# Kernel optimization log

Hardware: AMD Instinct MI355X
Metric: run time of the kernel (lower is better)

The kernel has to match this reference:

```python
import jax, jax.numpy as jnp
import numpy as np

IOU_THR = 0.5
SCORE_THR = 0.05
K = 1000  # fixed NMS candidate budget (padded-ragged replacement for data-dependent shapes)
BBOX_XFORM_CLIP = float(np.log(1000.0 / 16.0))  # torchvision BoxCoder clamp


def setup_inputs() -> dict:
    key = jax.random.key(0)
    k1, k2, k3, k4 = jax.random.split(key, 4)
    B, N, C = 8, 50000, 80
    pred_labels = jax.random.normal(k1, (B, N, C), jnp.float32)
    pred_bboxes = 0.5 * jax.random.normal(k2, (B, N, 4), jnp.float32)
    # anchors: valid xyxy boxes on a ~640px image
    cxy = jax.random.uniform(k3, (B, N, 2), jnp.float32, minval=0.0, maxval=640.0)
    wh = jax.random.uniform(k4, (B, N, 2), jnp.float32, minval=8.0, maxval=128.0)
    anchors = jnp.concatenate([cxy - 0.5 * wh, cxy + 0.5 * wh], axis=-1)
    return {"pred_labels": pred_labels, "pred_bboxes": pred_bboxes, "anchors": anchors}


def _decode_boxes(codes, anchors):
    # torchvision BoxCoder.decode_single with weights (1,1,1,1)
    w = anchors[:, 2] - anchors[:, 0]
    h = anchors[:, 3] - anchors[:, 1]
    cx = anchors[:, 0] + 0.5 * w
    cy = anchors[:, 1] + 0.5 * h
    dx, dy = codes[:, 0], codes[:, 1]
    dw = jnp.minimum(codes[:, 2], BBOX_XFORM_CLIP)
    dh = jnp.minimum(codes[:, 3], BBOX_XFORM_CLIP)
    pcx = dx * w + cx
    pcy = dy * h + cy
    pw = jnp.exp(dw) * w
    ph = jnp.exp(dh) * h
    return jnp.stack([pcx - 0.5 * pw, pcy - 0.5 * ph, pcx + 0.5 * pw, pcy + 0.5 * ph], axis=-1)


def _pairwise_iou(b):
    # b: [K,4] xyxy
    area = (b[:, 2] - b[:, 0]) * (b[:, 3] - b[:, 1])
    lt = jnp.maximum(b[:, None, :2], b[None, :, :2])
    rb = jnp.minimum(b[:, None, 2:], b[None, :, 2:])
    wh = jnp.clip(rb - lt, 0.0)
    inter = wh[..., 0] * wh[..., 1]
    return inter / (area[:, None] + area[None, :] - inter + 1e-9)


def _nms_keep(boxes):
    # boxes already sorted by descending score; greedy suppression
    iou = _pairwise_iou(boxes)
    idx = jnp.arange(K)

    def body(i, keep):
        suppress = (iou[i] > IOU_THR) & (idx > i) & keep[i]
        return keep & ~suppress

    return jax.lax.fori_loop(0, K, body, jnp.ones((K,), bool))


def _decode_image(labels, codes, anchors):
    # labels [N,C], codes [N,4], anchors [N,4]
    probs = jax.nn.sigmoid(labels)
    dt_score = jnp.max(probs, axis=1)
    dt_class = jnp.argmax(probs, axis=1)
    fg = (dt_class != 0) & (dt_score > SCORE_THR)
    masked = jnp.where(fg, dt_score, -1.0)  # background sorts last
    top_s, top_i = jax.lax.top_k(masked, K)
    cls = dt_class[top_i]
    boxes = _decode_boxes(codes[top_i], anchors[top_i])
    keep = _nms_keep(boxes) & (top_s > 0.0)
    out_scores = jnp.where(keep, top_s, 0.0)
    out_boxes = jnp.where(keep[:, None], boxes, 0.0)
    out_cls = jnp.where(keep, cls, -1)
    return out_cls, out_scores, out_boxes, keep


def reference(pred_labels, pred_bboxes, anchors):
    # Padded-ragged analog of the nested_tensor result:
    # category_ids [B,K] int, scores [B,K], bboxes [B,K,4], keep [B,K] validity mask
    return jax.vmap(_decode_image)(pred_labels, pred_bboxes, anchors)
```

## Files before the change

kernel.cpp:

```cpp
#include <hip/hip_runtime.h>
#include <cstdint>
#include <cstddef>

typedef unsigned int u32;
typedef unsigned long long u64;

#define BB   8
#define NN   50000
#define CC   80
#define KTOP 1000
#define CAP  4096
#define NHB  129
#define CLIPV 4.135166556742356f

#define OFF_KEYS 0UL
#define OFF_CLS  1600000UL
#define OFF_HIST 3200000UL
#define OFF_CNT  3204128UL
#define OFF_CAND 3204640UL
#define OFF_TKEY 3466784UL
#define OFF_TIDX 3498784UL
#define OFF_BOX  3530784UL
#define OFF_AREA 3658784UL
#define OFF_MAT  3690784UL
#define OFF_KEEP 4714784UL

__global__ __launch_bounds__(256) void k_scores_u(const float4* __restrict__ labels4,
                                                  u32* __restrict__ keys,
                                                  int* __restrict__ cls,
                                                  u32* __restrict__ ghist) {
    __shared__ float4 tile[64 * 21];
    __shared__ float  pbest[3][64];
    __shared__ int    pcls[3][64];
    __shared__ u32    lhist[NHB];
    int t = threadIdx.x;
    int img = blockIdx.x / 196;
    int blk = blockIdx.x - img * 196;
    size_t img_base = (size_t)img * NN * 20;
    for (int i = t; i < NHB; i += 256) lhist[i] = 0;
    int a = t & 63;
    int q = t >> 6;
#pragma unroll
    for (int tl = 0; tl < 4; ++tl) {
        int na0 = blk * 256 + tl * 64;
        int nv = NN - na0; if (nv > 64) nv = 64; if (nv < 0) nv = 0;
        int lim = nv * 20;
#pragma unroll
        for (int i = 0; i < 5; ++i) {
            int s = i * 256 + t;
            if (s < lim) {
                float4 v = labels4[img_base + (size_t)na0 * 20 + s];
                tile[s + s / 20] = v;
            }
        }
        __syncthreads();
        float best = -1.0e30f; int bc = 0;
        if (a < nv) {
#pragma unroll
            for (int j = 0; j < 5; ++j) {
                float4 v = tile[a * 21 + q * 5 + j];
                int c = q * 20 + j * 4;
                if (v.x > best) { best = v.x; bc = c; }
                if (v.y > best) { best = v.y; bc = c + 1; }
                if (v.z > best) { best = v.z; bc = c + 2; }
                if (v.w > best) { best = v.w; bc = c + 3; }
            }
            if (q > 0) { pbest[q - 1][a] = best; pcls[q - 1][a] = bc; }
        }
        __syncthreads();
        if (q == 0 && a < nv) {
#pragma unroll
            for (int r = 0; r < 3; ++r) {
                float pb = pbest[r][a];
                if (pb > best) { best = pb; bc = pcls[r][a]; }
            }
            int g = img * NN + na0 + a;
            float score = 1.0f / (1.0f + expf(-best));
            bool fg = (bc != 0) && (score > 0.05f);
            u32 key = fg ? __float_as_uint(score) : 0u;
            keys[g] = key;
            cls[g] = bc;
            u32 kb = key >> 16;
            u32 idx = (kb >= 0x3F00u) ? (kb - 0x3F00u) : 128u;
            atomicAdd(&lhist[idx], 1u);
        }
        __syncthreads();
    }
    for (int i = t; i < NHB; i += 256) {
        u32 c = lhist[i];
        if (c) atomicAdd(&ghist[img * NHB + i], c);
    }
}

__global__ __launch_bounds__(256) void k_gather(const u32* __restrict__ keys,
                                                const u32* __restrict__ ghist,
                                                u32* __restrict__ cnt,
                                                u64* __restrict__ cand) {
    __shared__ u32 wsum[4];
    __shared__ u32 bbase;
    __shared__ u32 sT16;
    __shared__ u32 wtot;
    int t = threadIdx.x;
    int img = blockIdx.x / 196;
    int blk = blockIdx.x - img * 196;

    u32 v = 0;
    if (t < 128) v = ghist[img * NHB + (127 - t)];
    u32 incl = v;
#pragma unroll
    for (int d = 1; d < 64; d <<= 1) {
        u32 up = __shfl_up(incl, (unsigned)d);
        if ((t & 63) >= d) incl += up;
    }
    if (t == 63) wtot = incl;
    __syncthreads();
    if (t >= 64 && t < 128) incl += wtot;
    if (t < 128) {
        u32 excl = incl - v;
        if (excl < KTOP && incl >= KTOP) sT16 = 0x3F00u + 127u - (u32)t;
    }
    if (t == 127 && incl < KTOP) sT16 = 0x3F00u;
    __syncthreads();
    u32 T16 = sT16;

    int n = blk * 256 + t;
    u32 key = 0; bool pass = false;
    if (n < NN) {
        key = keys[img * NN + n];
        pass = (key >> 16) >= T16;
    }
    u64 mask = __ballot(pass);
    int lane = t & 63, wid = t >> 6;
    u32 prefix = (u32)__popcll(mask & ((1ull << lane) - 1ull));
    if (lane == 0) wsum[wid] = (u32)__popcll(mask);
    __syncthreads();
    if (t == 0) {
        u32 s0 = wsum[0], s1 = wsum[1], s2 = wsum[2], s3 = wsum[3];
        u32 tot = s0 + s1 + s2 + s3;
        bbase = tot ? atomicAdd(&cnt[img * 16], tot) : 0u;
        wsum[0] = 0; wsum[1] = s0; wsum[2] = s0 + s1; wsum[3] = s0 + s1 + s2;
    }
    __syncthreads();
    if (pass) {
        u32 pos = bbase + wsum[wid] + prefix;
        if (pos < CAP)
            cand[(size_t)img * CAP + pos] = ((u64)key << 32) | (u32)(~(u32)n);
    }
}

__global__ __launch_bounds__(256) void k_sortA(u64* __restrict__ cand,
                                               const u32* __restrict__ cnt) {
    __shared__ u64 sm[1024];
    int b = blockIdx.x >> 2;
    int c = blockIdx.x & 3;
    int tid = threadIdx.x;
    int m = (int)min(cnt[b * 16], (u32)CAP);
    int base = c * 1024;
    u64* cp = cand + (size_t)b * CAP;
    for (int i = tid; i < 1024; i += 256) {
        int g = base + i;
        sm[i] = (g < m) ? cp[g] : 0ull;
    }
    __syncthreads();
    for (int k = 2; k <= 1024; k <<= 1)
        for (int j = k >> 1; j > 0; j >>= 1) {
            for (int i = tid; i < 1024; i += 256) {
                int ixj = i ^ j;
                if (ixj > i) {
                    bool desc = (((base + i) & k) == 0);
                    u64 x = sm[i], y = sm[ixj];
                    if (desc ? (x < y) : (x > y)) { sm[i] = y; sm[ixj] = x; }
                }
            }
            __syncthreads();
        }
    for (int i = tid; i < 1024; i += 256) cp[base + i] = sm[i];
}

__global__ __launch_bounds__(512) void k_sortB(const u64* __restrict__ cand,
                                               const float4* __restrict__ codes,
                                               const float4* __restrict__ anchors,
                                               u32* __restrict__ tkey, u32* __restrict__ tidx,
                                               float4* __restrict__ boxes, float* __restrict__ area) {
    __shared__ u64 sm[CAP];
    int b = blockIdx.x, tid = threadIdx.x;
    const u64* cp = cand + (size_t)b * CAP;
    for (int i = tid; i < CAP; i += 512) sm[i] = cp[i];
    __syncthreads();
    for (int k = 2048; k <= 4096; k <<= 1)
        for (int j = k >> 1; j > 0; j >>= 1) {
            for (int i = tid; i < CAP; i += 512) {
                int ixj = i ^ j;
                if (ixj > i) {
                    bool desc = ((i & k) == 0);
                    u64 x = sm[i], y = sm[ixj];
                    if (desc ? (x < y) : (x > y)) { sm[i] = y; sm[ixj] = x; }
                }
            }
            __syncthreads();
        }
#pragma unroll
    for (int r = 0; r < 2; ++r) {
        int i = r * 512 + tid;
        if (i < KTOP) {
            u64 v = sm[i];
            u32 kb = (u32)(v >> 32);
            u32 n = ~(u32)v;
            if (kb == 0u) n = 0u;
            int g = b * KTOP + i;
            tkey[g] = kb; tidx[g] = n;
            float4 a = anchors[(size_t)b * NN + n];
            float4 cc = codes[(size_t)b * NN + n];
            float w = a.z - a.x, h = a.w - a.y;
            float cx = a.x + 0.5f * w, cy = a.y + 0.5f * h;
            float dw = fminf(cc.z, CLIPV), dh = fminf(cc.w, CLIPV);
            float pcx = cc.x * w + cx, pcy = cc.y * h + cy;
            float pw = expf(dw) * w, ph = expf(dh) * h;
            float x0 = pcx - 0.5f * pw, y0 = pcy - 0.5f * ph;
            float x1 = pcx + 0.5f * pw, y1 = pcy + 0.5f * ph;
            boxes[g] = make_float4(x0, y0, x1, y1);
            area[g] = (x1 - x0) * (y1 - y0);
        }
    }
}

__global__ __launch_bounds__(256) void k_mat(const float4* __restrict__ boxes,
                                             const float* __restrict__ area,
                                             u64* __restrict__ mat) {
    __shared__ float4 sb[256];
    __shared__ float  sa[256];
    int bid = blockIdx.x;
    int wc = bid & 3, rc = (bid >> 2) & 3, b = bid >> 4;
    int t = threadIdx.x;
    int j0 = wc * 256;
    int jn = min(256, KTOP - j0);
    if (t < jn) { sb[t] = boxes[b * KTOP + j0 + t]; sa[t] = area[b * KTOP + j0 + t]; }
    __syncthreads();
    if (t >= 250) return;
    int i = rc * 250 + t;
    float4 bi = boxes[b * KTOP + i];
    float ai = area[b * KTOP + i];
    u64 w[4] = {0ull, 0ull, 0ull, 0ull};
    int estart = i - j0 + 1; if (estart < 0) estart = 0;
    for (int e = estart; e < jn; ++e) {
        float4 bj = sb[e];
        float lx = fmaxf(bi.x, bj.x), ly = fmaxf(bi.y, bj.y);
        float rx = fminf(bi.z, bj.z), ry = fminf(bi.w, bj.w);
        float ww = fmaxf(rx - lx, 0.0f), hh = fmaxf(ry - ly, 0.0f);
        float inter = ww * hh;
        float iou = inter / (ai + sa[e] - inter + 1e-9f);
        if (iou > 0.5f) w[e >> 6] |= (1ull << (e & 63));
    }
    u64* outp = &mat[((size_t)(b * KTOP + i)) * 16 + wc * 4];
    outp[0] = w[0]; outp[1] = w[1]; outp[2] = w[2]; outp[3] = w[3];
}

__global__ __launch_bounds__(64) void k_nms2(const u64* __restrict__ mat,
                                             u64* __restrict__ keepw) {
    int b = blockIdx.x, lane = threadIdx.x;
    const u64* mb = mat + (size_t)b * (KTOP * 16);
    u64 kw[16];
#pragma unroll
    for (int w = 0; w < 15; ++w) kw[w] = ~0ull;
    kw[15] = (1ull << 40) - 1;
    for (int p = 0; p < 16; ++p) {
        int row = p * 64 + lane;
        u64 r[16];
        if (row < KTOP) {
            const u64* rp = mb + (size_t)row * 16;
#pragma unroll
            for (int w = 0; w < 16; ++w) r[w] = rp[w];
        } else {
#pragma unroll
            for (int w = 0; w < 16; ++w) r[w] = 0ull;
        }
        u64 kwp = kw[p];
        u64 applied = 0;
        u64 myp = r[p];
#pragma unroll 1
        for (int e = 0; e < 64; ++e) {
            if ((kwp >> e) & 1ull) {
                u64 s = __shfl(myp, e);
                kwp &= ~s;
                applied |= (1ull << e);
            }
        }
        kw[p] = kwp;
        bool mine = (applied >> lane) & 1ull;
        for (int w = p + 1; w < 16; ++w) {
            u64 v = mine ? r[w] : 0ull;
#pragma unroll
            for (int d = 32; d > 0; d >>= 1) v |= __shfl_xor(v, d);
            kw[w] &= ~v;
        }
    }
    if (lane < 16) keepw[b * 16 + lane] = kw[lane];
}

__global__ __launch_bounds__(256) void k_out(const u64* __restrict__ keepw,
                                             const u32* __restrict__ tkey,
                                             const u32* __restrict__ tidx,
                                             const int* __restrict__ cls,
                                             const float4* __restrict__ boxes,
                                             float* __restrict__ out) {
    int gid = blockIdx.x * 256 + threadIdx.x;
    if (gid >= BB * KTOP) return;
    int b = gid / KTOP;
    int k = gid - b * KTOP;
    u64 kwv = keepw[b * 16 + (k >> 6)];
    bool kp = (kwv >> (k & 63)) & 1ull;
    float sc = __uint_as_float(tkey[gid]);
    kp = kp && (sc > 0.0f);
    int cl = cls[(size_t)b * NN + tidx[gid]];
    float4 bx = boxes[gid];
    const int BK = BB * KTOP;
    out[gid] = kp ? (float)cl : -1.0f;
    out[BK + gid] = kp ? sc : 0.0f;
    float* ob = out + 2 * BK + (size_t)gid * 4;
    ob[0] = kp ? bx.x : 0.0f;
    ob[1] = kp ? bx.y : 0.0f;
    ob[2] = kp ? bx.z : 0.0f;
    ob[3] = kp ? bx.w : 0.0f;
    out[6 * BK + gid] = kp ? 1.0f : 0.0f;
}

extern "C" void kernel_launch(void* const* d_in, const int* in_sizes, int n_in,
                              void* d_out, int out_size, void* d_ws, size_t ws_size,
                              hipStream_t stream) {
    const float* labels  = (const float*)d_in[0];
    const float* codes   = (const float*)d_in[1];
    const float* anchors = (const float*)d_in[2];
    char* ws = (char*)d_ws;
    u32* keys  = (u32*)(ws + OFF_KEYS);
    int* cls   = (int*)(ws + OFF_CLS);
    u32* hist  = (u32*)(ws + OFF_HIST);
    u32* cnt   = (u32*)(ws + OFF_CNT);
    u64* cand  = (u64*)(ws + OFF_CAND);
    u32* tkey  = (u32*)(ws + OFF_TKEY);
    u32* tidx  = (u32*)(ws + OFF_TIDX);
    float4* bx = (float4*)(ws + OFF_BOX);
    float* ar  = (float*)(ws + OFF_AREA);
    u64* mat   = (u64*)(ws + OFF_MAT);
    u64* kpw   = (u64*)(ws + OFF_KEEP);

    hipMemsetAsync(ws + OFF_HIST, 0, OFF_CAND - OFF_HIST, stream);

    k_scores_u<<<BB * 196, 256, 0, stream>>>((const float4*)labels, keys, cls, hist);
    k_gather<<<BB * 196, 256, 0, stream>>>(keys, hist, cnt, cand);
    k_sortA<<<BB * 4, 256, 0, stream>>>(cand, cnt);
    k_sortB<<<BB, 512, 0, stream>>>(cand, (const float4*)codes, (const float4*)anchors,
                                    tkey, tidx, bx, ar);
    k_mat<<<BB * 16, 256, 0, stream>>>(bx, ar, mat);
    k_nms2<<<BB, 64, 0, stream>>>(mat, kpw);
    k_out<<<(BB * KTOP + 255) / 256, 256, 0, stream>>>(kpw, tkey, tidx, cls, bx, (float*)d_out);
}
```

Before: 435.2 us.

## Transpose IoU bitmask layout and resolve NMS blocks via ballot fixpoint iteration

The suppression matrix is now stored transposed, by column word then row word then lane, so that each lane owns one candidate and reads a coalesced 64-bit mask of its suppressors. The greedy NMS kernel drops the serial 64-step shuffle loop per diagonal block and computes the surviving set with an iterated ballot fixpoint. Cross-block suppression becomes a per-lane AND against the alive set instead of shuffle-xor reductions. The fixpoint can take many iterations when suppression chains are long, and the matrix kernel now has each thread handle a column j with a triangular loop.

New measurement: 361.2 us. 17.0% less time.

```diff
diff --git a/kernel.cpp b/kernel.cpp
--- a/kernel.cpp
+++ b/kernel.cpp
@@ -22,8 +22,8 @@
 #define OFF_TIDX 3498784UL
 #define OFF_BOX  3530784UL
 #define OFF_AREA 3658784UL
-#define OFF_MAT  3690784UL
-#define OFF_KEEP 4714784UL
+#define OFF_MATT 3690784UL
+#define OFF_KEEP 4739360UL
 
 __global__ __launch_bounds__(256) void k_scores_u(const float4* __restrict__ labels4,
                                                   u32* __restrict__ keys,
@@ -224,77 +224,70 @@
     }
 }
 
-__global__ __launch_bounds__(256) void k_mat(const float4* __restrict__ boxes,
-                                             const float* __restrict__ area,
-                                             u64* __restrict__ mat) {
+__global__ __launch_bounds__(256) void k_matT(const float4* __restrict__ boxes,
+                                              const float* __restrict__ area,
+                                              u64* __restrict__ matT) {
     __shared__ float4 sb[256];
     __shared__ float  sa[256];
     int bid = blockIdx.x;
-    int wc = bid & 3, rc = (bid >> 2) & 3, b = bid >> 4;
+    int rw = bid & 3, cc = (bid >> 2) & 3, b = bid >> 4;
     int t = threadIdx.x;
-    int j0 = wc * 256;
-    int jn = min(256, KTOP - j0);
-    if (t < jn) { sb[t] = boxes[b * KTOP + j0 + t]; sa[t] = area[b * KTOP + j0 + t]; }
-    __syncthreads();
-    if (t >= 250) return;
-    int i = rc * 250 + t;
-    float4 bi = boxes[b * KTOP + i];
-    float ai = area[b * KTOP + i];
+    int i0 = rw * 256;
+    int in_ = min(256, KTOP - i0);
+    if (t < in_) { sb[t] = boxes[b * KTOP + i0 + t]; sa[t] = area[b * KTOP + i0 + t]; }
+    __syncthreads();
+    int j = cc * 256 + t;
     u64 w[4] = {0ull, 0ull, 0ull, 0ull};
-    int estart = i - j0 + 1; if (estart < 0) estart = 0;
-    for (int e = estart; e < jn; ++e) {
-        float4 bj = sb[e];
-        float lx = fmaxf(bi.x, bj.x), ly = fmaxf(bi.y, bj.y);
-        float rx = fminf(bi.z, bj.z), ry = fminf(bi.w, bj.w);
-        float ww = fmaxf(rx - lx, 0.0f), hh = fmaxf(ry - ly, 0.0f);
-        float inter = ww * hh;
-        float iou = inter / (ai + sa[e] - inter + 1e-9f);
-        if (iou > 0.5f) w[e >> 6] |= (1ull << (e & 63));
-    }
-    u64* outp = &mat[((size_t)(b * KTOP + i)) * 16 + wc * 4];
-    outp[0] = w[0]; outp[1] = w[1]; outp[2] = w[2]; outp[3] = w[3];
-}
-
-__global__ __launch_bounds__(64) void k_nms2(const u64* __restrict__ mat,
+    if (j < KTOP) {
+        float4 bj = boxes[b * KTOP + j];
+        float aj = area[b * KTOP + j];
+        int emax = j - i0; if (emax > in_) emax = in_;
+        for (int e = 0; e < emax; ++e) {
+            float4 bi = sb[e];
+            float lx = fmaxf(bi.x, bj.x), ly = fmaxf(bi.y, bj.y);
+            float rx = fminf(bi.z, bj.z), ry = fminf(bi.w, bj.w);
+            float ww = fmaxf(rx - lx, 0.0f), hh = fmaxf(ry - ly, 0.0f);
+            float inter = ww * hh;
+            float iou = inter / (sa[e] + aj - inter + 1e-9f);
+            if (iou > 0.5f) w[e >> 6] |= (1ull << (e & 63));
+        }
+    }
+    int wcol = cc * 4 + (t >> 6);
+    int lane = t & 63;
+    u64* outp = matT + (size_t)b * (16 * 16 * 64);
+#pragma unroll
+    for (int lw = 0; lw < 4; ++lw)
+        outp[((size_t)wcol * 16 + (rw * 4 + lw)) * 64 + lane] = w[lw];
+}
+
+__global__ __launch_bounds__(64) void k_nms3(const u64* __restrict__ matT,
                                              u64* __restrict__ keepw) {
-    int b = blockIdx.x, lane = threadIdx.x;
-    const u64* mb = mat + (size_t)b * (KTOP * 16);
-    u64 kw[16];
-#pragma unroll
-    for (int w = 0; w < 15; ++w) kw[w] = ~0ull;
-    kw[15] = (1ull << 40) - 1;
+    int b = blockIdx.x, l = threadIdx.x;
+    const u64* mt = matT + (size_t)b * (16 * 16 * 64);
+    u32 keepmask = (l < 40) ? 0xFFFFu : 0x7FFFu;
     for (int p = 0; p < 16; ++p) {
-        int row = p * 64 + lane;
-        u64 r[16];
-        if (row < KTOP) {
-            const u64* rp = mb + (size_t)row * 16;
-#pragma unroll
-            for (int w = 0; w < 16; ++w) r[w] = rp[w];
-        } else {
-#pragma unroll
-            for (int w = 0; w < 16; ++w) r[w] = 0ull;
-        }
-        u64 kwp = kw[p];
-        u64 applied = 0;
-        u64 myp = r[p];
-#pragma unroll 1
-        for (int e = 0; e < 64; ++e) {
-            if ((kwp >> e) & 1ull) {
-                u64 s = __shfl(myp, e);
-                kwp &= ~s;
-                applied |= (1ull << e);
-            }
-        }
-        kw[p] = kwp;
-        bool mine = (applied >> lane) & 1ull;
+        u64 diag = mt[((size_t)p * 16 + p) * 64 + l];
+        bool init = (keepmask >> p) & 1u;
+        u64 aset = __ballot(init);
+        for (;;) {
+            bool alive = init && !(diag & aset);
+            u64 ns = __ballot(alive);
+            if (ns == aset) break;
+            aset = ns;
+        }
+        keepmask = (keepmask & ~(1u << p)) | ((u32)((aset >> l) & 1ull) << p);
         for (int w = p + 1; w < 16; ++w) {
-            u64 v = mine ? r[w] : 0ull;
-#pragma unroll
-            for (int d = 32; d > 0; d >>= 1) v |= __shfl_xor(v, d);
-            kw[w] &= ~v;
-        }
-    }
-    if (lane < 16) keepw[b * 16 + lane] = kw[lane];
+            u64 cm = mt[((size_t)w * 16 + p) * 64 + l];
+            if (cm & aset) keepmask &= ~(1u << w);
+        }
+    }
+    u64 word = 0;
+#pragma unroll
+    for (int w = 0; w < 16; ++w) {
+        u64 bw = __ballot((keepmask >> w) & 1u);
+        if (l == w) word = bw;
+    }
+    if (l < 16) keepw[b * 16 + l] = word;
 }
 
 __global__ __launch_bounds__(256) void k_out(const u64* __restrict__ keepw,
@@ -340,7 +333,7 @@
     u32* tidx  = (u32*)(ws + OFF_TIDX);
     float4* bx = (float4*)(ws + OFF_BOX);
     float* ar  = (float*)(ws + OFF_AREA);
-    u64* mat   = (u64*)(ws + OFF_MAT);
+    u64* mtt   = (u64*)(ws + OFF_MATT);
     u64* kpw   = (u64*)(ws + OFF_KEEP);
 
     hipMemsetAsync(ws + OFF_HIST, 0, OFF_CAND - OFF_HIST, stream);
@@ -350,7 +343,7 @@
     k_sortA<<<BB * 4, 256, 0, stream>>>(cand, cnt);
     k_sortB<<<BB, 512, 0, stream>>>(cand, (const float4*)codes, (const float4*)anchors,
                                     tkey, tidx, bx, ar);
-    k_mat<<<BB * 16, 256, 0, stream>>>(bx, ar, mat);
-    k_nms2<<<BB, 64, 0, stream>>>(mat, kpw);
+    k_matT<<<BB * 16, 256, 0, stream>>>(bx, ar, mtt);
+    k_nms3<<<BB, 64, 0, stream>>>(mtt, kpw);
     k_out<<<(BB * KTOP + 255) / 256, 256, 0, stream>>>(kpw, tkey, tidx, cls, bx, (float*)d_out);
 }
```
